# Performance work log

Measured on AMD Instinct MI355X. Metric: run time of the kernel, lower is better.

Reference implementation:

```python
import jax, jax.numpy as jnp
import numpy as np

B, T, I, H, O = 32, 2048, 12, 512, 3
L = 3  # GRU layers


def _gru_layer(x_seq, h0, w_ih, w_hh, b_ih, b_hh):
    # x_seq: [B,T,D], h0: [B,H]; PyTorch gate order: r, z, n
    xW = jnp.einsum('btd,gd->btg', x_seq, w_ih) + b_ih  # [B,T,3H]

    def step(h, xw_t):
        hw = h @ w_hh.T + b_hh                  # [B,3H]
        xr, xz, xn = jnp.split(xw_t, 3, axis=-1)
        hr, hz, hn = jnp.split(hw, 3, axis=-1)
        r = jax.nn.sigmoid(xr + hr)
        z = jax.nn.sigmoid(xz + hz)
        n = jnp.tanh(xn + r * hn)
        h_new = (1.0 - z) * n + z * h
        return h_new, h_new

    h_last, ys = jax.lax.scan(step, h0, jnp.swapaxes(xW, 0, 1))  # ys: [T,B,H]
    return jnp.swapaxes(ys, 0, 1), h_last


def _prelu(x, a):
    return jnp.where(x >= 0, x, a * x)


def setup_inputs() -> dict:
    key = jax.random.key(0)
    ks = jax.random.split(key, 40)
    s = 1.0 / np.sqrt(H)

    def u(k, shape):
        return jax.random.uniform(k, shape, jnp.float32, -s, s)

    inp = {
        'x': jax.random.normal(ks[0], (B, T, I), jnp.float32),
        'vel_init': jax.random.normal(ks[1], (B, 1, 3), jnp.float32),
    }
    in_dims = [I, H, H]
    for l in range(L):
        inp[f'w_ih_{l}'] = u(ks[2 + 4 * l], (3 * H, in_dims[l]))
        inp[f'w_hh_{l}'] = u(ks[3 + 4 * l], (3 * H, H))
        inp[f'b_ih_{l}'] = u(ks[4 + 4 * l], (3 * H,))
        inp[f'b_hh_{l}'] = u(ks[5 + 4 * l], (3 * H,))
    inp['a1'] = jnp.array([0.25], jnp.float32)  # PReLU (single shared param)
    inp['dec_in_w'] = u(ks[14], (H, I)); inp['dec_in_b'] = u(ks[15], (H,))
    inp['vd0_w'] = u(ks[16], (H, 3)); inp['vd0_b'] = u(ks[17], (H,))
    inp['vd1_w'] = u(ks[18], (H, 3)); inp['vd1_b'] = u(ks[19], (H,))
    inp['vd2_w'] = u(ks[20], (H, 3)); inp['vd2_b'] = u(ks[21], (H,))
    inp['vel_w'] = u(ks[22], (O, H)); inp['vel_b'] = u(ks[23], (O,))
    inp['std_w'] = u(ks[24], (O, H)); inp['std_b'] = u(ks[25], (O,))
    inp['attn_w'] = u(ks[26], (1, H)); inp['attn_b'] = u(ks[27], (1,))
    return inp


def reference(x, vel_init, w_ih_0, w_hh_0, b_ih_0, b_hh_0,
              w_ih_1, w_hh_1, b_ih_1, b_hh_1,
              w_ih_2, w_hh_2, b_ih_2, b_hh_2,
              a1, dec_in_w, dec_in_b,
              vd0_w, vd0_b, vd1_w, vd1_b, vd2_w, vd2_b,
              vel_w, vel_b, std_w, std_b, attn_w, attn_b):
    v0 = vel_init[:, 0, :]  # [B,3]
    # h0 per layer from velocity decoders (permute(1,0,2)+cat -> layer axis)
    h0s = [v0 @ vd0_w.T + vd0_b, v0 @ vd1_w.T + vd1_b, v0 @ vd2_w.T + vd2_b]
    w_ih = [w_ih_0, w_ih_1, w_ih_2]
    w_hh = [w_hh_0, w_hh_1, w_hh_2]
    b_ih = [b_ih_0, b_ih_1, b_ih_2]
    b_hh = [b_hh_0, b_hh_1, b_hh_2]

    out = x
    for l in range(L):
        out, _ = _gru_layer(out, h0s[l], w_ih[l], w_hh[l], b_ih[l], b_hh[l])

    out = _prelu(out, a1)
    # softmax skip-attention over time dim
    scores = jnp.einsum('bth,oh->bto', out, attn_w) + attn_b      # [B,T,1]
    attn = jax.nn.softmax(scores, axis=1)
    out = out + attn * (jnp.einsum('bti,hi->bth', x, dec_in_w) + dec_in_b)

    vel = jnp.einsum('bth,oh->bto', out, vel_w) + vel_b
    std = jnp.einsum('bth,oh->bto', out, std_w) + std_b
    return vel, std
```

## Files before the change

### kernel.cpp

```cpp
#include <hip/hip_runtime.h>
#include <stdint.h>


#define B_ 32
#define T_ 2048
#define H_ 512
#define R_ 128

typedef __attribute__((ext_vector_type(8))) short s8v;
typedef __attribute__((ext_vector_type(4))) float f4v;
typedef __attribute__((ext_vector_type(4))) uint32_t u32x4;
typedef __attribute__((ext_vector_type(2))) unsigned short u16x2;

__device__ __forceinline__ uint16_t f2bf(float f){ return __builtin_bit_cast(uint16_t, (__bf16)f); }
__device__ __forceinline__ float bf2f(uint16_t b){ return __builtin_bit_cast(float, ((uint32_t)b)<<16); }

__device__ __forceinline__ s8v pack8(const float* f){
  s8v r;
  #pragma unroll
  for (int i=0;i<8;++i) r[i] = (short)f2bf(f[i]);
  return r;
}
__device__ __forceinline__ f4v mfma16(s8v a, s8v b, f4v c){
  return __builtin_amdgcn_mfma_f32_16x16x32_bf16(a,b,c,0,0,0);
}
#if __has_builtin(__builtin_amdgcn_rcpf)
__device__ __forceinline__ float rcp_(float x){ return __builtin_amdgcn_rcpf(x); }
#else
__device__ __forceinline__ float rcp_(float x){ return 1.0f/x; }
#endif
__device__ __forceinline__ float sigm(float s){ return rcp_(1.f + __expf(-s)); }
__device__ __forceinline__ float tanh2(float v){ return 1.f - 2.f*rcp_(1.f + __expf(2.f*v)); }

__device__ __forceinline__ u32x4 load_x4_sc(const void* p){
  u32x4 r;
  asm volatile("global_load_dwordx4 %0, %1, off sc0 sc1" : "=v"(r) : "v"(p) : "memory");
  return r;
}
__device__ __forceinline__ u32x4 load_x4_sc_wait(const void* p){
  u32x4 r;
  asm volatile("global_load_dwordx4 %0, %1, off sc0 sc1\n\ts_waitcnt vmcnt(0)"
               : "=v"(r) : "v"(p) : "memory");
  return r;
}
__device__ __forceinline__ uint32_t load_u32_sc_wait(const void* p){
  uint32_t r;
  asm volatile("global_load_dword %0, %1, off sc0 sc1\n\ts_waitcnt vmcnt(0)"
               : "=v"(r) : "v"(p) : "memory");
  return r;
}
__device__ __forceinline__ void store_s16_sc(void* p, uint32_t v){
  asm volatile("global_store_short %0, %1, off sc0 sc1" :: "v"(p), "v"(v) : "memory");
}
__device__ __forceinline__ void store_u32_sc(void* p, uint32_t v){
  asm volatile("global_store_dword %0, %1, off sc0 sc1" :: "v"(p), "v"(v) : "memory");
}

__device__ __forceinline__ bool chunk_ok(u32x4 c){
  u16x2 m = __builtin_bit_cast(u16x2, c[0]);
  m = __builtin_elementwise_max(m, __builtin_bit_cast(u16x2, c[1]));
  m = __builtin_elementwise_max(m, __builtin_bit_cast(u16x2, c[2]));
  m = __builtin_elementwise_max(m, __builtin_bit_cast(u16x2, c[3]));
  unsigned short mm = (m[0] > m[1]) ? m[0] : m[1];
  return mm != (unsigned short)0xFFFFu;
}
__device__ __forceinline__ bool valid16(const u32x4* a){
  u16x2 m = {0, 0};
  #pragma unroll
  for (int c=0;c<16;++c){
    #pragma unroll
    for (int i=0;i<4;++i)
      m = __builtin_elementwise_max(m, __builtin_bit_cast(u16x2, a[c][i]));
  }
  unsigned short mm = (m[0] > m[1]) ? m[0] : m[1];
  return mm != (unsigned short)0xFFFFu;
}

__global__ void poison_kernel(uint32_t* p, unsigned int n16)
{
  u32x4 v = {0xFFFFFFFFu, 0xFFFFFFFFu, 0xFFFFFFFFu, 0xFFFFFFFFu};
  for (unsigned int k = blockIdx.x*blockDim.x + threadIdx.x; k < n16;
       k += gridDim.x*blockDim.x)
    ((u32x4*)p)[k] = v;
}

__global__ void init_kernel(const float* __restrict__ vel_init,
    const float* __restrict__ w0, const float* __restrict__ b0,
    const float* __restrict__ w1, const float* __restrict__ b1,
    const float* __restrict__ w2, const float* __restrict__ b2,
    float* __restrict__ h0f, uint16_t* __restrict__ h0b, uint32_t* progress)
{
  const int l = blockIdx.x, tid = threadIdx.x;
  const float* w  = (l==0)?w0:((l==1)?w1:w2);
  const float* bb = (l==0)?b0:((l==1)?b1:b2);
  for (int idx = tid; idx < B_*H_; idx += 256){
    int b = idx >> 9, j = idx & 511;
    float s = bb[j] + vel_init[b*3+0]*w[j*3+0] + vel_init[b*3+1]*w[j*3+1]
                    + vel_init[b*3+2]*w[j*3+2];
    h0f[(size_t)l*(B_*H_) + idx] = s;
    h0b[(size_t)l*(B_*H_) + idx] = f2bf(s);
  }
  if (l == 0 && tid < 192) progress[tid] = 0;
}

struct ScanParams {
  const float* x;
  const float* wih[3];
  const float* whh[3];
  const float* bih[3];
  const float* bhh[3];
  const float* h0f;
  const uint16_t* h0b;
  uint16_t* ring0;
  uint16_t* ring1;
  uint16_t* out2;
  uint32_t* progress;
};

__global__ __launch_bounds__(128, 1) void fused_scan(ScanParams P)
{
  const int tid  = threadIdx.x;
  const int lane = tid & 63;
  const int mt   = tid >> 6;
  const int wgid = blockIdx.x;
  const int layer = wgid >> 5;
  const int wg   = wgid & 31;
  const int j0   = wg * 16;
  const int u    = lane & 15;
  const int lq   = lane >> 4;
  const int ko   = lq * 8;
  const int bd   = lq * 4;

  __shared__ uint16_t lds[48*512];

  const float* wih = P.wih[layer];
  const float* whh = P.whh[layer];
  const float* bih = P.bih[layer];
  const float* bhh = P.bhh[layer];

  const float bs0 = bih[0*H_ + j0 + u] + bhh[0*H_ + j0 + u];
  const float bs1 = bih[1*H_ + j0 + u] + bhh[1*H_ + j0 + u];
  const float bi2 = bih[2*H_ + j0 + u];
  const float bh2 = bhh[2*H_ + j0 + u];

  s8v whhf[3][16];
  #pragma unroll
  for (int nt=0; nt<3; ++nt){
    #pragma unroll
    for (int ks=0; ks<16; ++ks){
      const float* wp = whh + (size_t)(nt*H_ + j0 + u)*H_ + ks*32 + ko;
      float tmp[8];
      #pragma unroll
      for (int i=0;i<8;++i) tmp[i] = wp[i];
      whhf[nt][ks] = pack8(tmp);
    }
  }

  s8v w0f[3];
  if (layer == 0){
    #pragma unroll
    for (int nt=0; nt<3; ++nt){
      float tmp[8];
      #pragma unroll
      for (int i=0;i<8;++i){
        int k = ko + i;
        tmp[i] = (k < 12) ? wih[(size_t)(nt*H_ + j0 + u)*12 + k] : 0.f;
      }
      w0f[nt] = pack8(tmp);
    }
  } else {
    for (int e = tid; e < (48*512)/8; e += 128) {
      int idx = e * 8;
      int g = idx >> 9, k = idx & 511;
      const float* wp = wih + (size_t)((g>>4)*H_ + j0 + (g&15))*H_ + k;
      float tmp[8];
      #pragma unroll
      for (int i=0;i<8;++i) tmp[i] = wp[i];
      s8v v = pack8(tmp);
      uint32_t msk = (uint32_t)((((g&7) ^ (((g>>3)&1)<<1))) << 4);
      uint32_t off = (uint32_t)g*1024u + ((((uint32_t)k)*2u) ^ msk);
      *(u32x4*)((char*)lds + off) = __builtin_bit_cast(u32x4, v);
    }
  }
  __syncthreads();

  const uint16_t* inring = (layer==1) ? P.ring0 : P.ring1;
  uint16_t* outbuf = (layer==0) ? P.ring0 : ((layer==1) ? P.ring1 : P.out2);
  const bool outlin = (layer == 2);
  uint32_t* myprog = P.progress + layer*64 + wg*2 + mt;
  const uint32_t* nextprog = (layer<2) ? (P.progress + (layer+1)*64) : nullptr;

  float hold[4];
  #pragma unroll
  for (int r=0;r<4;++r)
    hold[r] = P.h0f[(size_t)layer*(B_*H_) + (size_t)(mt*16 + bd + r)*H_ + j0 + u];

  const uint32_t sw  = (uint32_t)((((u&7) ^ (((u>>3)&1)<<1))) << 4);
  const uint32_t gb0 = (uint32_t)((0*16 + u) * 1024);
  const uint32_t gb1 = (uint32_t)((1*16 + u) * 1024);
  const uint32_t gb2 = (uint32_t)((2*16 + u) * 1024);
  const uint32_t koB = (uint32_t)(ko * 2);
  const int cl = lane & 31;

  int poison_until = R_/2 - 4;

  for (int t = 0; t < T_; ++t) {
    f4v ac0 = {0,0,0,0}, ac1 = {0,0,0,0}, axn = {0,0,0,0}, ahn = {0,0,0,0};

    if (layer == 0) {
      const float* xp = P.x + ((size_t)(mt*16 + u)*T_ + (size_t)t)*12;
      float4 lo  = *(const float4*)(xp);
      float4 md  = *(const float4*)(xp + 4);
      float4 hi4 = *(const float4*)(xp + 8);
      float xv[8];
      xv[0] = (ko==0) ? lo.x : hi4.x;  xv[1] = (ko==0) ? lo.y : hi4.y;
      xv[2] = (ko==0) ? lo.z : hi4.z;  xv[3] = (ko==0) ? lo.w : hi4.w;
      xv[4] = (ko==0) ? md.x : 0.f;    xv[5] = (ko==0) ? md.y : 0.f;
      xv[6] = (ko==0) ? md.z : 0.f;    xv[7] = (ko==0) ? md.w : 0.f;
      s8v a = pack8(xv);
      ac0 = mfma16(a, w0f[0], ac0);
      ac1 = mfma16(a, w0f[1], ac1);
      axn = mfma16(a, w0f[2], axn);
    } else {
      const uint16_t* xslot = inring + (size_t)(t & (R_-1))*(B_*H_);
      const uint16_t* xin  = xslot + (size_t)(mt*16+u)*H_ + ko;
      const uint16_t* xcan = xslot + (size_t)(mt*16)*H_ + cl*16;
      u32x4 xa[16];
      while (1) {
        #pragma unroll
        for (int ks=0; ks<16; ++ks) xa[ks] = load_x4_sc(xin + ks*32);
        asm volatile("s_waitcnt vmcnt(0)" ::: "memory");
        __builtin_amdgcn_sched_barrier(0);
        if (__ballot(valid16(xa)) == ~0ull) break;
        while (1) {
          u32x4 c = load_x4_sc_wait(xcan);
          if (__ballot(chunk_ok(c)) == ~0ull) break;
          __builtin_amdgcn_s_sleep(2);
        }
      }
      #pragma unroll
      for (int ks=0; ks<16; ++ks){
        s8v a = __builtin_bit_cast(s8v, xa[ks]);
        uint32_t kk = ((uint32_t)(ks*64) + koB) ^ sw;
        s8v w0 = *(const s8v*)((const char*)lds + gb0 + kk);
        s8v w1 = *(const s8v*)((const char*)lds + gb1 + kk);
        s8v w2 = *(const s8v*)((const char*)lds + gb2 + kk);
        ac0 = mfma16(a, w0, ac0);
        ac1 = mfma16(a, w1, ac1);
        axn = mfma16(a, w2, axn);
      }
    }

    const uint16_t* hslot = (t == 0)
        ? (P.h0b + (size_t)layer*(B_*H_))
        : (outlin ? (P.out2 + (size_t)(t-1)*(B_*H_))
                  : (outbuf + (size_t)((t-1) & (R_-1))*(B_*H_)));
    const uint16_t* hp   = hslot + (size_t)(mt*16+u)*H_ + ko;
    const uint16_t* hcan = hslot + (size_t)(mt*16)*H_ + cl*16;
    u32x4 ha[16];
    while (1) {
      #pragma unroll
      for (int ks=0; ks<16; ++ks) ha[ks] = load_x4_sc(hp + ks*32);
      asm volatile("s_waitcnt vmcnt(0)" ::: "memory");
      __builtin_amdgcn_sched_barrier(0);
      if (t == 0) break;
      if (__ballot(valid16(ha)) == ~0ull) break;
      while (1) {
        u32x4 c = load_x4_sc_wait(hcan);
        if (__ballot(chunk_ok(c)) == ~0ull) break;
        __builtin_amdgcn_s_sleep(2);
      }
    }
    #pragma unroll
    for (int ks=0; ks<16; ++ks){
      s8v a = __builtin_bit_cast(s8v, ha[ks]);
      ac0 = mfma16(a, whhf[0][ks], ac0);
      ac1 = mfma16(a, whhf[1][ks], ac1);
      ahn = mfma16(a, whhf[2][ks], ahn);
    }

    uint16_t* orow = outbuf
        + (outlin ? (size_t)t*(B_*H_) : (size_t)(t & (R_-1))*(B_*H_))
        + (size_t)(mt*16 + bd)*H_ + j0 + u;
    #pragma unroll
    for (int r=0;r<4;++r){
      float rg = sigm(ac0[r] + bs0);
      float zg = sigm(ac1[r] + bs1);
      float ng = tanh2(axn[r] + bi2 + rg*(ahn[r] + bh2));
      float hv = ng + zg*(hold[r] - ng);
      hold[r] = hv;
      store_s16_sc(orow + (size_t)r*H_, (uint32_t)f2bf(hv));
    }

    if (layer > 0 && (t & 15) == 15 && lane == 0)
      store_u32_sc(myprog, (uint32_t)t);

    if (layer < 2 && t >= R_/2) {
      if (t > poison_until) {
        while (1) {
          int c = (int)load_u32_sc_wait(nextprog + lane);
          #pragma unroll
          for (int off=32; off>0; off>>=1){
            int c2 = __shfl_xor(c, off, 64);
            c = (c2 < c) ? c2 : c;
          }
          poison_until = c + R_/2 - 4;
          if (t <= poison_until) break;
          __builtin_amdgcn_s_sleep(8);
        }
      }
      int sp = (t + R_/2) & (R_-1);
      uint16_t* prow = outbuf + (size_t)sp*(B_*H_) + (size_t)(mt*16 + bd)*H_ + j0 + u;
      #pragma unroll
      for (int r=0;r<4;++r) store_s16_sc(prow + (size_t)r*H_, 0xFFFFu);
    }
  }
}

__global__ void scores_kernel(const uint16_t* __restrict__ out2,
    const float* __restrict__ attn_w, const float* __restrict__ attn_b,
    const float* __restrict__ a1, float* __restrict__ scores)
{
  int gw = (blockIdx.x * blockDim.x + threadIdx.x) >> 6;
  int lane = threadIdx.x & 63;
  int b = gw >> 11, t = gw & 2047;
  float alpha = a1[0];
  u32x4 q = *(const u32x4*)(out2 + ((size_t)t*B_ + b)*H_ + lane*8);
  const uint16_t* ob = (const uint16_t*)&q;
  const float* aw = attn_w + lane*8;
  float acc = 0.f;
  #pragma unroll
  for (int i=0;i<8;++i){
    float ov = bf2f(ob[i]);
    ov = (ov >= 0.f) ? ov : alpha*ov;
    acc += ov * aw[i];
  }
  #pragma unroll
  for (int off=32; off>0; off>>=1) acc += __shfl_xor(acc, off, 64);
  if (lane == 0) scores[(size_t)b*T_ + t] = acc + attn_b[0];
}

__global__ void softmax_kernel(const float* __restrict__ scores, float* __restrict__ attn)
{
  int b = blockIdx.x, tid = threadIdx.x;
  __shared__ float red[256];
  const float* row = scores + (size_t)b*T_;
  float v[8]; float m = -3.4e38f;
  #pragma unroll
  for (int i=0;i<8;++i){ v[i] = row[tid + i*256]; m = fmaxf(m, v[i]); }
  red[tid] = m; __syncthreads();
  for (int s=128; s>0; s>>=1){ if (tid < s) red[tid] = fmaxf(red[tid], red[tid+s]); __syncthreads(); }
  m = red[0]; __syncthreads();
  float sum = 0.f;
  #pragma unroll
  for (int i=0;i<8;++i){ v[i] = __expf(v[i]-m); sum += v[i]; }
  red[tid] = sum; __syncthreads();
  for (int s=128; s>0; s>>=1){ if (tid < s) red[tid] += red[tid+s]; __syncthreads(); }
  float inv = 1.f / red[0];
  #pragma unroll
  for (int i=0;i<8;++i) attn[(size_t)b*T_ + tid + i*256] = v[i]*inv;
}

__global__ void final_kernel(const uint16_t* __restrict__ out2, const float* __restrict__ x,
    const float* __restrict__ attn, const float* __restrict__ dw, const float* __restrict__ db,
    const float* __restrict__ vw, const float* __restrict__ vb,
    const float* __restrict__ swt, const float* __restrict__ sb,
    const float* __restrict__ a1, float* __restrict__ dout)
{
  int gw = (blockIdx.x * blockDim.x + threadIdx.x) >> 6;
  int lane = threadIdx.x & 63;
  int b = gw >> 11, t = gw & 2047;
  float alpha = a1[0];
  u32x4 q = *(const u32x4*)(out2 + ((size_t)t*B_ + b)*H_ + lane*8);
  const uint16_t* ob = (const uint16_t*)&q;
  const float* xp = x + ((size_t)b*T_ + t)*12;
  float xr[12];
  #pragma unroll
  for (int i=0;i<12;++i) xr[i] = xp[i];
  float av = attn[(size_t)b*T_ + t];
  float acc[6] = {0,0,0,0,0,0};
  #pragma unroll
  for (int k=0;k<8;++k){
    int j = lane*8 + k;
    float ov = bf2f(ob[k]);
    ov = (ov >= 0.f) ? ov : alpha*ov;
    float d = db[j];
    const float* dwp = dw + (size_t)j*12;
    #pragma unroll
    for (int i=0;i<12;++i) d += xr[i]*dwp[i];
    float uo = ov + av*d;
    #pragma unroll
    for (int o=0;o<3;++o){
      acc[o]   += uo * vw[(size_t)o*H_ + j];
      acc[3+o] += uo * swt[(size_t)o*H_ + j];
    }
  }
  #pragma unroll
  for (int o=0;o<6;++o){
    #pragma unroll
    for (int off=32; off>0; off>>=1) acc[o] += __shfl_xor(acc[o], off, 64);
  }
  if (lane == 0){
    size_t p = ((size_t)b*T_ + t)*3;
    #pragma unroll
    for (int o=0;o<3;++o){
      dout[p + o] = acc[o] + vb[o];
      dout[(size_t)B_*T_*3 + p + o] = acc[3+o] + sb[o];
    }
  }
}

extern "C" void kernel_launch(void* const* d_in, const int* in_sizes, int n_in,
                              void* d_out, int out_size, void* d_ws, size_t ws_size,
                              hipStream_t stream)
{
  (void)in_sizes; (void)n_in; (void)out_size; (void)ws_size;
  const float* x        = (const float*)d_in[0];
  const float* vel_init = (const float*)d_in[1];
  const float* w_ih[3] = {(const float*)d_in[2], (const float*)d_in[6],  (const float*)d_in[10]};
  const float* w_hh[3] = {(const float*)d_in[3], (const float*)d_in[7],  (const float*)d_in[11]};
  const float* b_ih[3] = {(const float*)d_in[4], (const float*)d_in[8],  (const float*)d_in[12]};
  const float* b_hh[3] = {(const float*)d_in[5], (const float*)d_in[9],  (const float*)d_in[13]};
  const float* a1     = (const float*)d_in[14];
  const float* dec_w  = (const float*)d_in[15];
  const float* dec_b  = (const float*)d_in[16];
  const float* vd_w[3] = {(const float*)d_in[17], (const float*)d_in[19], (const float*)d_in[21]};
  const float* vd_b[3] = {(const float*)d_in[18], (const float*)d_in[20], (const float*)d_in[22]};
  const float* vel_w  = (const float*)d_in[23];
  const float* vel_b  = (const float*)d_in[24];
  const float* std_w  = (const float*)d_in[25];
  const float* std_b  = (const float*)d_in[26];
  const float* attn_w = (const float*)d_in[27];
  const float* attn_b = (const float*)d_in[28];

  char* ws = (char*)d_ws;
  uint16_t* out2   = (uint16_t*)(ws);
  uint16_t* ring0  = (uint16_t*)(ws + (size_t)67108864);
  uint16_t* ring1  = (uint16_t*)(ws + (size_t)71303168);
  float*    h0f    = (float*)   (ws + (size_t)75497472);
  uint16_t* h0b    = (uint16_t*)(ws + (size_t)75694080);
  float*    scores = (float*)   (ws + (size_t)75792384);
  float*    attnp  = (float*)   (ws + (size_t)76054528);
  uint32_t* progress = (uint32_t*)(ws + (size_t)76316672);

  poison_kernel<<<2048, 256, 0, stream>>>((uint32_t*)ws, 72u*1024u*1024u/16u);
  init_kernel<<<3, 256, 0, stream>>>(vel_init, vd_w[0], vd_b[0], vd_w[1], vd_b[1],
                                     vd_w[2], vd_b[2], h0f, h0b, progress);

  ScanParams P;
  P.x = x;
  for (int l=0;l<3;++l){ P.wih[l]=w_ih[l]; P.whh[l]=w_hh[l]; P.bih[l]=b_ih[l]; P.bhh[l]=b_hh[l]; }
  P.h0f = h0f; P.h0b = h0b;
  P.ring0 = ring0; P.ring1 = ring1; P.out2 = out2; P.progress = progress;

  fused_scan<<<96, 128, 0, stream>>>(P);

  scores_kernel<<<(B_*T_)/4, 256, 0, stream>>>(out2, attn_w, attn_b, a1, scores);
  softmax_kernel<<<B_, 256, 0, stream>>>(scores, attnp);
  final_kernel<<<(B_*T_)/4, 256, 0, stream>>>(out2, x, attnp, dec_w, dec_b,
                                              vel_w, vel_b, std_w, std_b, a1, (float*)d_out);
}
```

Baseline: 8.427 ms.

## Pin each GRU layer to its own XCD and use L2-scoped recurrent exchange

Launches extra workgroups and has each one read its XCC id and claim a layer slot through atomics, so that all 32 workgroups of a layer share one XCD. When every layer lands on its home XCD, the per-step hidden-state exchange uses an 8-deep ring with L2-scoped (sc0) loads and stores instead of system-coherent ones. The next timestep's input activations are also prefetched during the current step. Surplus workgroups exit early. The cost is a startup claim/barrier phase, reliance on XCC placement, and a spin fallback to coherent loads if workgroups end up off their home XCD.

New measurement: 8.520 ms. Within noise of the previous version (+1.1%).

```diff
diff --git a/kernel.cpp b/kernel.cpp
--- a/kernel.cpp
+++ b/kernel.cpp
@@ -6,6 +6,7 @@
 #define T_ 2048
 #define H_ 512
 #define R_ 128
+#define HR_ 8
 
 typedef __attribute__((ext_vector_type(8))) short s8v;
 typedef __attribute__((ext_vector_type(4))) float f4v;
@@ -55,6 +56,24 @@
 __device__ __forceinline__ void store_u32_sc(void* p, uint32_t v){
   asm volatile("global_store_dword %0, %1, off sc0 sc1" :: "v"(p), "v"(v) : "memory");
 }
+__device__ __forceinline__ u32x4 load_x4_l2(const void* p){
+  u32x4 r;
+  asm volatile("global_load_dwordx4 %0, %1, off sc0" : "=v"(r) : "v"(p) : "memory");
+  return r;
+}
+__device__ __forceinline__ void store_s16_l2(void* p, uint32_t v){
+  asm volatile("global_store_short %0, %1, off sc0" :: "v"(p), "v"(v) : "memory");
+}
+
+__device__ __forceinline__ void load16(u32x4* a, const uint16_t* base, bool l2){
+  if (l2) {
+    #pragma unroll
+    for (int ks=0; ks<16; ++ks) a[ks] = load_x4_l2(base + ks*32);
+  } else {
+    #pragma unroll
+    for (int ks=0; ks<16; ++ks) a[ks] = load_x4_sc(base + ks*32);
+  }
+}
 
 __device__ __forceinline__ bool chunk_ok(u32x4 c){
   u16x2 m = __builtin_bit_cast(u16x2, c[0]);
@@ -76,6 +95,17 @@
   return mm != (unsigned short)0xFFFFu;
 }
 
+__device__ __forceinline__ uint32_t get_xcc(){
+  uint32_t x;
+  asm volatile("s_getreg_b32 %0, hwreg(HW_REG_XCC_ID)" : "=s"(x));
+  return x & 7u;
+}
+__device__ __forceinline__ uint64_t realtime_(){
+  uint64_t t;
+  asm volatile("s_memrealtime %0\n\ts_waitcnt lgkmcnt(0)" : "=s"(t));
+  return t;
+}
+
 __global__ void poison_kernel(uint32_t* p, unsigned int n16)
 {
   u32x4 v = {0xFFFFFFFFu, 0xFFFFFFFFu, 0xFFFFFFFFu, 0xFFFFFFFFu};
@@ -88,7 +118,8 @@
     const float* __restrict__ w0, const float* __restrict__ b0,
     const float* __restrict__ w1, const float* __restrict__ b1,
     const float* __restrict__ w2, const float* __restrict__ b2,
-    float* __restrict__ h0f, uint16_t* __restrict__ h0b, uint32_t* progress)
+    float* __restrict__ h0f, uint16_t* __restrict__ h0b,
+    uint32_t* progress, uint32_t* claimp)
 {
   const int l = blockIdx.x, tid = threadIdx.x;
   const float* w  = (l==0)?w0:((l==1)?w1:w2);
@@ -101,6 +132,7 @@
     h0b[(size_t)l*(B_*H_) + idx] = f2bf(s);
   }
   if (l == 0 && tid < 192) progress[tid] = 0;
+  if (l == 0 && tid >= 192 && tid < 200) claimp[tid-192] = 0;
 }
 
 struct ScanParams {
@@ -111,10 +143,13 @@
   const float* bhh[3];
   const float* h0f;
   const uint16_t* h0b;
-  uint16_t* ring0;
-  uint16_t* ring1;
+  uint16_t* xr0;
+  uint16_t* xr1;
+  uint16_t* hr0;
+  uint16_t* hr1;
   uint16_t* out2;
   uint32_t* progress;
+  uint32_t* claimp;
 };
 
 __global__ __launch_bounds__(128, 1) void fused_scan(ScanParams P)
@@ -122,16 +157,59 @@
   const int tid  = threadIdx.x;
   const int lane = tid & 63;
   const int mt   = tid >> 6;
-  const int wgid = blockIdx.x;
-  const int layer = wgid >> 5;
-  const int wg   = wgid & 31;
-  const int j0   = wg * 16;
   const int u    = lane & 15;
   const int lq   = lane >> 4;
   const int ko   = lq * 8;
   const int bd   = lq * 4;
 
   __shared__ uint16_t lds[48*512];
+  __shared__ char pad_[36864];
+  __shared__ int sh_role[3];
+  if (P.x == nullptr) ((volatile char*)pad_)[0] = 1;
+
+  if (tid == 0){
+    int layer = -1, wg = -1, home = 0;
+    uint32_t xcc = get_xcc();
+    if (xcc < 3u){
+      unsigned s = atomicAdd(&P.claimp[xcc], 1u);
+      if (s < 32u){ layer = (int)xcc; wg = (int)s; home = 1; }
+    }
+    if (layer < 0){
+      uint64_t t0 = realtime_();
+      while (realtime_() - t0 < 5000ull) __builtin_amdgcn_s_sleep(32);
+      for (;;){
+        bool allfull = true;
+        for (int l=0; l<3 && layer<0; ++l){
+          if (__hip_atomic_load(&P.claimp[l], __ATOMIC_RELAXED,
+                                __HIP_MEMORY_SCOPE_AGENT) < 32u){
+            allfull = false;
+            unsigned s = atomicAdd(&P.claimp[l], 1u);
+            if (s < 32u){ layer = l; wg = (int)s; home = (xcc == (uint32_t)l); }
+          }
+        }
+        if (layer >= 0 || allfull) break;
+        __builtin_amdgcn_s_sleep(16);
+      }
+    }
+    int fast = 0;
+    if (layer >= 0){
+      if (!home) atomicAdd(&P.claimp[4], 1u);
+      __hip_atomic_fetch_add(&P.claimp[3], 1u, __ATOMIC_ACQ_REL,
+                             __HIP_MEMORY_SCOPE_AGENT);
+      while (__hip_atomic_load(&P.claimp[3], __ATOMIC_ACQUIRE,
+                               __HIP_MEMORY_SCOPE_AGENT) < 96u)
+        __builtin_amdgcn_s_sleep(8);
+      fast = (__hip_atomic_load(&P.claimp[4], __ATOMIC_ACQUIRE,
+                                __HIP_MEMORY_SCOPE_AGENT) == 0u) ? 1 : 0;
+    }
+    sh_role[0] = layer; sh_role[1] = wg; sh_role[2] = fast;
+  }
+  __syncthreads();
+  const int layer = sh_role[0];
+  if (layer < 0) return;
+  const int wg = sh_role[1];
+  const bool fastmode = (sh_role[2] != 0);
+  const int j0 = wg * 16;
 
   const float* wih = P.wih[layer];
   const float* whh = P.whh[layer];
@@ -184,9 +262,9 @@
   }
   __syncthreads();
 
-  const uint16_t* inring = (layer==1) ? P.ring0 : P.ring1;
-  uint16_t* outbuf = (layer==0) ? P.ring0 : ((layer==1) ? P.ring1 : P.out2);
-  const bool outlin = (layer == 2);
+  const uint16_t* inring = (layer==1) ? P.xr0 : P.xr1;
+  uint16_t* hring = (layer==0) ? P.hr0 : P.hr1;
+  uint16_t* xout  = (layer==0) ? P.xr0 : P.xr1;
   uint32_t* myprog = P.progress + layer*64 + wg*2 + mt;
   const uint32_t* nextprog = (layer<2) ? (P.progress + (layer+1)*64) : nullptr;
 
@@ -201,11 +279,49 @@
   const uint32_t gb2 = (uint32_t)((2*16 + u) * 1024);
   const uint32_t koB = (uint32_t)(ko * 2);
   const int cl = lane & 31;
-
-  int poison_until = R_/2 - 4;
+  const size_t rowoff = (size_t)(mt*16 + bd)*H_ + j0 + u;
+
+  bool hfast = fastmode;
+  int poison_until = 63;
+
+  u32x4 xa[16];
+  auto issue_x = [&](int tt){
+    const uint16_t* xin = inring + (size_t)(tt & (R_-1))*(B_*H_)
+                          + (size_t)(mt*16+u)*H_ + ko;
+    #pragma unroll
+    for (int ks=0; ks<16; ++ks) xa[ks] = load_x4_sc(xin + ks*32);
+  };
+  if (layer > 0) issue_x(0);
 
   for (int t = 0; t < T_; ++t) {
     f4v ac0 = {0,0,0,0}, ac1 = {0,0,0,0}, axn = {0,0,0,0}, ahn = {0,0,0,0};
+
+    if (layer > 0) {
+      asm volatile("s_waitcnt vmcnt(0)" ::: "memory");
+      __builtin_amdgcn_sched_barrier(0);
+      if (__ballot(valid16(xa)) != ~0ull) {
+        const uint16_t* xslot = inring + (size_t)(t & (R_-1))*(B_*H_);
+        const uint16_t* xcan  = xslot + (size_t)(mt*16)*H_ + cl*16;
+        do {
+          while (1) {
+            u32x4 c = load_x4_sc_wait(xcan);
+            if (__ballot(chunk_ok(c)) == ~0ull) break;
+            __builtin_amdgcn_s_sleep(2);
+          }
+          issue_x(t);
+          asm volatile("s_waitcnt vmcnt(0)" ::: "memory");
+          __builtin_amdgcn_sched_barrier(0);
+        } while (__ballot(valid16(xa)) != ~0ull);
+      }
+    }
+
+    const uint16_t* hsrc = (t == 0)
+        ? (P.h0b + (size_t)layer*(B_*H_))
+        : (layer == 2 ? (P.out2 + (size_t)(t-1)*(B_*H_))
+                      : (hring + (size_t)((t-1) & (HR_-1))*(B_*H_)));
+    const uint16_t* hp = hsrc + (size_t)(mt*16+u)*H_ + ko;
+    u32x4 ha[16];
+    load16(ha, hp, hfast);
 
     if (layer == 0) {
       const float* xp = P.x + ((size_t)(mt*16 + u)*T_ + (size_t)t)*12;
@@ -222,22 +338,6 @@
       ac1 = mfma16(a, w0f[1], ac1);
       axn = mfma16(a, w0f[2], axn);
     } else {
-      const uint16_t* xslot = inring + (size_t)(t & (R_-1))*(B_*H_);
-      const uint16_t* xin  = xslot + (size_t)(mt*16+u)*H_ + ko;
-      const uint16_t* xcan = xslot + (size_t)(mt*16)*H_ + cl*16;
-      u32x4 xa[16];
-      while (1) {
-        #pragma unroll
-        for (int ks=0; ks<16; ++ks) xa[ks] = load_x4_sc(xin + ks*32);
-        asm volatile("s_waitcnt vmcnt(0)" ::: "memory");
-        __builtin_amdgcn_sched_barrier(0);
-        if (__ballot(valid16(xa)) == ~0ull) break;
-        while (1) {
-          u32x4 c = load_x4_sc_wait(xcan);
-          if (__ballot(chunk_ok(c)) == ~0ull) break;
-          __builtin_amdgcn_s_sleep(2);
-        }
-      }
       #pragma unroll
       for (int ks=0; ks<16; ++ks){
         s8v a = __builtin_bit_cast(s8v, xa[ks]);
@@ -251,26 +351,19 @@
       }
     }
 
-    const uint16_t* hslot = (t == 0)
-        ? (P.h0b + (size_t)layer*(B_*H_))
-        : (outlin ? (P.out2 + (size_t)(t-1)*(B_*H_))
-                  : (outbuf + (size_t)((t-1) & (R_-1))*(B_*H_)));
-    const uint16_t* hp   = hslot + (size_t)(mt*16+u)*H_ + ko;
-    const uint16_t* hcan = hslot + (size_t)(mt*16)*H_ + cl*16;
-    u32x4 ha[16];
-    while (1) {
-      #pragma unroll
-      for (int ks=0; ks<16; ++ks) ha[ks] = load_x4_sc(hp + ks*32);
-      asm volatile("s_waitcnt vmcnt(0)" ::: "memory");
-      __builtin_amdgcn_sched_barrier(0);
-      if (t == 0) break;
-      if (__ballot(valid16(ha)) == ~0ull) break;
-      while (1) {
-        u32x4 c = load_x4_sc_wait(hcan);
-        if (__ballot(chunk_ok(c)) == ~0ull) break;
-        __builtin_amdgcn_s_sleep(2);
-      }
-    }
+    asm volatile("s_waitcnt vmcnt(0)" ::: "memory");
+    __builtin_amdgcn_sched_barrier(0);
+    if (t > 0) {
+      int spins = 0;
+      while (__ballot(valid16(ha)) != ~0ull) {
+        if (++spins > 512) hfast = false;
+        __builtin_amdgcn_s_sleep(1);
+        load16(ha, hp, hfast);
+        asm volatile("s_waitcnt vmcnt(0)" ::: "memory");
+        __builtin_amdgcn_sched_barrier(0);
+      }
+    }
+
     #pragma unroll
     for (int ks=0; ks<16; ++ks){
       s8v a = __builtin_bit_cast(s8v, ha[ks]);
@@ -279,23 +372,46 @@
       ahn = mfma16(a, whhf[2][ks], ahn);
     }
 
-    uint16_t* orow = outbuf
-        + (outlin ? (size_t)t*(B_*H_) : (size_t)(t & (R_-1))*(B_*H_))
-        + (size_t)(mt*16 + bd)*H_ + j0 + u;
-    #pragma unroll
-    for (int r=0;r<4;++r){
-      float rg = sigm(ac0[r] + bs0);
-      float zg = sigm(ac1[r] + bs1);
-      float ng = tanh2(axn[r] + bi2 + rg*(ahn[r] + bh2));
-      float hv = ng + zg*(hold[r] - ng);
-      hold[r] = hv;
-      store_s16_sc(orow + (size_t)r*H_, (uint32_t)f2bf(hv));
+    if (layer < 2) {
+      uint16_t* hrow = hring + (size_t)(t & (HR_-1))*(B_*H_) + rowoff;
+      uint16_t* xrow = xout  + (size_t)(t & (R_-1))*(B_*H_) + rowoff;
+      #pragma unroll
+      for (int r=0;r<4;++r){
+        float rg = sigm(ac0[r] + bs0);
+        float zg = sigm(ac1[r] + bs1);
+        float ng = tanh2(axn[r] + bi2 + rg*(ahn[r] + bh2));
+        float hv = ng + zg*(hold[r] - ng);
+        hold[r] = hv;
+        uint32_t bv = (uint32_t)f2bf(hv);
+        if (fastmode) store_s16_l2(hrow + (size_t)r*H_, bv);
+        else          store_s16_sc(hrow + (size_t)r*H_, bv);
+        store_s16_sc(xrow + (size_t)r*H_, bv);
+      }
+      uint16_t* prow = hring + (size_t)((t+4) & (HR_-1))*(B_*H_) + rowoff;
+      #pragma unroll
+      for (int r=0;r<4;++r){
+        if (fastmode) store_s16_l2(prow + (size_t)r*H_, 0xFFFFu);
+        else          store_s16_sc(prow + (size_t)r*H_, 0xFFFFu);
+      }
+    } else {
+      uint16_t* orow = P.out2 + (size_t)t*(B_*H_) + rowoff;
+      #pragma unroll
+      for (int r=0;r<4;++r){
+        float rg = sigm(ac0[r] + bs0);
+        float zg = sigm(ac1[r] + bs1);
+        float ng = tanh2(axn[r] + bi2 + rg*(ahn[r] + bh2));
+        float hv = ng + zg*(hold[r] - ng);
+        hold[r] = hv;
+        uint32_t bv = (uint32_t)f2bf(hv);
+        if (fastmode) store_s16_l2(orow + (size_t)r*H_, bv);
+        else          store_s16_sc(orow + (size_t)r*H_, bv);
+      }
     }
 
     if (layer > 0 && (t & 15) == 15 && lane == 0)
       store_u32_sc(myprog, (uint32_t)t);
 
-    if (layer < 2 && t >= R_/2) {
+    if (layer < 2 && t >= 64) {
       if (t > poison_until) {
         while (1) {
           int c = (int)load_u32_sc_wait(nextprog + lane);
@@ -304,16 +420,17 @@
             int c2 = __shfl_xor(c, off, 64);
             c = (c2 < c) ? c2 : c;
           }
-          poison_until = c + R_/2 - 4;
+          poison_until = c + 60;
           if (t <= poison_until) break;
           __builtin_amdgcn_s_sleep(8);
         }
       }
-      int sp = (t + R_/2) & (R_-1);
-      uint16_t* prow = outbuf + (size_t)sp*(B_*H_) + (size_t)(mt*16 + bd)*H_ + j0 + u;
-      #pragma unroll
-      for (int r=0;r<4;++r) store_s16_sc(prow + (size_t)r*H_, 0xFFFFu);
-    }
+      uint16_t* qrow = xout + (size_t)((t+64) & (R_-1))*(B_*H_) + rowoff;
+      #pragma unroll
+      for (int r=0;r<4;++r) store_s16_sc(qrow + (size_t)r*H_, 0xFFFFu);
+    }
+
+    if (layer > 0 && t+1 < T_) issue_x(t+1);
   }
 }
 
@@ -435,25 +552,29 @@
 
   char* ws = (char*)d_ws;
   uint16_t* out2   = (uint16_t*)(ws);
-  uint16_t* ring0  = (uint16_t*)(ws + (size_t)67108864);
-  uint16_t* ring1  = (uint16_t*)(ws + (size_t)71303168);
-  float*    h0f    = (float*)   (ws + (size_t)75497472);
-  uint16_t* h0b    = (uint16_t*)(ws + (size_t)75694080);
-  float*    scores = (float*)   (ws + (size_t)75792384);
-  float*    attnp  = (float*)   (ws + (size_t)76054528);
-  uint32_t* progress = (uint32_t*)(ws + (size_t)76316672);
-
-  poison_kernel<<<2048, 256, 0, stream>>>((uint32_t*)ws, 72u*1024u*1024u/16u);
+  uint16_t* xr0    = (uint16_t*)(ws + (size_t)67108864);
+  uint16_t* xr1    = (uint16_t*)(ws + (size_t)71303168);
+  uint16_t* hr0    = (uint16_t*)(ws + (size_t)75497472);
+  uint16_t* hr1    = (uint16_t*)(ws + (size_t)75759616);
+  float*    h0f    = (float*)   (ws + (size_t)76021760);
+  uint16_t* h0b    = (uint16_t*)(ws + (size_t)76218368);
+  float*    scores = (float*)   (ws + (size_t)76316672);
+  float*    attnp  = (float*)   (ws + (size_t)76578816);
+  uint32_t* progress = (uint32_t*)(ws + (size_t)76840960);
+  uint32_t* claimp   = (uint32_t*)(ws + (size_t)76841728);
+
+  poison_kernel<<<2048, 256, 0, stream>>>((uint32_t*)ws, 76021760u/16u);
   init_kernel<<<3, 256, 0, stream>>>(vel_init, vd_w[0], vd_b[0], vd_w[1], vd_b[1],
-                                     vd_w[2], vd_b[2], h0f, h0b, progress);
+                                     vd_w[2], vd_b[2], h0f, h0b, progress, claimp);
 
   ScanParams P;
   P.x = x;
   for (int l=0;l<3;++l){ P.wih[l]=w_ih[l]; P.whh[l]=w_hh[l]; P.bih[l]=b_ih[l]; P.bhh[l]=b_hh[l]; }
   P.h0f = h0f; P.h0b = h0b;
-  P.ring0 = ring0; P.ring1 = ring1; P.out2 = out2; P.progress = progress;
-
-  fused_scan<<<96, 128, 0, stream>>>(P);
+  P.xr0 = xr0; P.xr1 = xr1; P.hr0 = hr0; P.hr1 = hr1;
+  P.out2 = out2; P.progress = progress; P.claimp = claimp;
+
+  fused_scan<<<256, 128, 0, stream>>>(P);
 
   scores_kernel<<<(B_*T_)/4, 256, 0, stream>>>(out2, attn_w, attn_b, a1, scores);
   softmax_kernel<<<B_, 256, 0, stream>>>(scores, attnp);
```

## Prefetch next-step h/x loads speculatively and batch stores via LDS transpose

Applied to the files above, without the earlier changes.

Each step's h-state and layer-input loads are now issued right after the previous step's gates are computed, so they overlap with the output store and the poison and progress handling instead of starting at the top of the next step. The workgroup's own freshly computed h slice is merged from LDS so it does not wait on a global round trip. Outputs are transposed through a small LDS buffer so each lane writes one dwordx2 in place of four scattered 16-bit stores, and poison writes are batched the same way. The speculative loads may read not-yet-valid (poisoned) data and then fall back to the poll-and-reload path, which adds retry traffic when the prefetch runs ahead of the producers.

New measurement: 11.37 ms. +34.9%, slower.

```diff
diff --git a/kernel.cpp b/kernel.cpp
--- a/kernel.cpp
+++ b/kernel.cpp
@@ -6,10 +6,12 @@
 #define T_ 2048
 #define H_ 512
 #define R_ 128
+#define BH_ (B_*H_)
 
 typedef __attribute__((ext_vector_type(8))) short s8v;
 typedef __attribute__((ext_vector_type(4))) float f4v;
 typedef __attribute__((ext_vector_type(4))) uint32_t u32x4;
+typedef __attribute__((ext_vector_type(2))) uint32_t u32x2;
 typedef __attribute__((ext_vector_type(2))) unsigned short u16x2;
 
 __device__ __forceinline__ uint16_t f2bf(float f){ return __builtin_bit_cast(uint16_t, (__bf16)f); }
@@ -49,8 +51,8 @@
                : "=v"(r) : "v"(p) : "memory");
   return r;
 }
-__device__ __forceinline__ void store_s16_sc(void* p, uint32_t v){
-  asm volatile("global_store_short %0, %1, off sc0 sc1" :: "v"(p), "v"(v) : "memory");
+__device__ __forceinline__ void store_x2_sc(void* p, u32x2 v){
+  asm volatile("global_store_dwordx2 %0, %1, off sc0 sc1" :: "v"(p), "v"(v) : "memory");
 }
 __device__ __forceinline__ void store_u32_sc(void* p, uint32_t v){
   asm volatile("global_store_dword %0, %1, off sc0 sc1" :: "v"(p), "v"(v) : "memory");
@@ -97,8 +99,8 @@
     int b = idx >> 9, j = idx & 511;
     float s = bb[j] + vel_init[b*3+0]*w[j*3+0] + vel_init[b*3+1]*w[j*3+1]
                     + vel_init[b*3+2]*w[j*3+2];
-    h0f[(size_t)l*(B_*H_) + idx] = s;
-    h0b[(size_t)l*(B_*H_) + idx] = f2bf(s);
+    h0f[(size_t)l*BH_ + idx] = s;
+    h0b[(size_t)l*BH_ + idx] = f2bf(s);
   }
   if (l == 0 && tid < 192) progress[tid] = 0;
 }
@@ -132,6 +134,7 @@
   const int bd   = lq * 4;
 
   __shared__ uint16_t lds[48*512];
+  __shared__ uint16_t lds_t[2][2][16][16];
 
   const float* wih = P.wih[layer];
   const float* whh = P.whh[layer];
@@ -193,7 +196,7 @@
   float hold[4];
   #pragma unroll
   for (int r=0;r<4;++r)
-    hold[r] = P.h0f[(size_t)layer*(B_*H_) + (size_t)(mt*16 + bd + r)*H_ + j0 + u];
+    hold[r] = P.h0f[(size_t)layer*BH_ + (size_t)(mt*16 + bd + r)*H_ + j0 + u];
 
   const uint32_t sw  = (uint32_t)((((u&7) ^ (((u>>3)&1)<<1))) << 4);
   const uint32_t gb0 = (uint32_t)((0*16 + u) * 1024);
@@ -201,17 +204,54 @@
   const uint32_t gb2 = (uint32_t)((2*16 + u) * 1024);
   const uint32_t koB = (uint32_t)(ko * 2);
   const int cl = lane & 31;
+  const int sb = lane >> 2, sq = lane & 3;
+  const size_t wrow = (size_t)(mt*16 + sb)*H_ + j0 + sq*4;
+  const int ks0 = wg >> 1;
+  const bool ownseg = ((lq >> 1) == (wg & 1));
 
   int poison_until = R_/2 - 4;
 
+  u32x4 ha[16], xa[16], x0a[3];
+  const uint16_t* hp = P.h0b + (size_t)layer*BH_ + (size_t)(mt*16+u)*H_ + ko;
+
+  auto hload = [&](){
+    #pragma unroll
+    for (int ks=0; ks<16; ++ks) ha[ks] = load_x4_sc(hp + ks*32);
+  };
+  auto issue_x = [&](int tt){
+    const uint16_t* xin = inring + (size_t)(tt & (R_-1))*BH_
+                          + (size_t)(mt*16+u)*H_ + ko;
+    #pragma unroll
+    for (int ks=0; ks<16; ++ks) xa[ks] = load_x4_sc(xin + ks*32);
+  };
+  auto issue_x0 = [&](int tt){
+    const float* xp = P.x + ((size_t)(mt*16 + u)*T_ + (size_t)tt)*12;
+    x0a[0] = *(const u32x4*)(xp);
+    x0a[1] = *(const u32x4*)(xp + 4);
+    x0a[2] = *(const u32x4*)(xp + 8);
+  };
+  auto merge_own = [&](int p){
+    u32x4 own = *(const u32x4*)&lds_t[p][mt][u][(lq & 1) * 8];
+    if (ownseg) {
+      #pragma unroll
+      for (int ks=0; ks<16; ++ks)
+        if (ks == ks0) ha[ks] = own;
+    }
+  };
+
+  hload();
+  if (layer == 0) issue_x0(0); else issue_x(0);
+
   for (int t = 0; t < T_; ++t) {
+    asm volatile("s_waitcnt vmcnt(0)" ::: "memory");
+    __builtin_amdgcn_sched_barrier(0);
+
     f4v ac0 = {0,0,0,0}, ac1 = {0,0,0,0}, axn = {0,0,0,0}, ahn = {0,0,0,0};
 
     if (layer == 0) {
-      const float* xp = P.x + ((size_t)(mt*16 + u)*T_ + (size_t)t)*12;
-      float4 lo  = *(const float4*)(xp);
-      float4 md  = *(const float4*)(xp + 4);
-      float4 hi4 = *(const float4*)(xp + 8);
+      float4 lo  = __builtin_bit_cast(float4, x0a[0]);
+      float4 md  = __builtin_bit_cast(float4, x0a[1]);
+      float4 hi4 = __builtin_bit_cast(float4, x0a[2]);
       float xv[8];
       xv[0] = (ko==0) ? lo.x : hi4.x;  xv[1] = (ko==0) ? lo.y : hi4.y;
       xv[2] = (ko==0) ? lo.z : hi4.z;  xv[3] = (ko==0) ? lo.w : hi4.w;
@@ -222,21 +262,19 @@
       ac1 = mfma16(a, w0f[1], ac1);
       axn = mfma16(a, w0f[2], axn);
     } else {
-      const uint16_t* xslot = inring + (size_t)(t & (R_-1))*(B_*H_);
-      const uint16_t* xin  = xslot + (size_t)(mt*16+u)*H_ + ko;
-      const uint16_t* xcan = xslot + (size_t)(mt*16)*H_ + cl*16;
-      u32x4 xa[16];
-      while (1) {
-        #pragma unroll
-        for (int ks=0; ks<16; ++ks) xa[ks] = load_x4_sc(xin + ks*32);
-        asm volatile("s_waitcnt vmcnt(0)" ::: "memory");
-        __builtin_amdgcn_sched_barrier(0);
-        if (__ballot(valid16(xa)) == ~0ull) break;
-        while (1) {
-          u32x4 c = load_x4_sc_wait(xcan);
-          if (__ballot(chunk_ok(c)) == ~0ull) break;
-          __builtin_amdgcn_s_sleep(2);
-        }
+      if (__ballot(valid16(xa)) != ~0ull) {
+        const uint16_t* xslot = inring + (size_t)(t & (R_-1))*BH_;
+        const uint16_t* xcan  = xslot + (size_t)(mt*16)*H_ + cl*16;
+        do {
+          while (1) {
+            u32x4 c = load_x4_sc_wait(xcan);
+            if (__ballot(chunk_ok(c)) == ~0ull) break;
+            __builtin_amdgcn_s_sleep(2);
+          }
+          issue_x(t);
+          asm volatile("s_waitcnt vmcnt(0)" ::: "memory");
+          __builtin_amdgcn_sched_barrier(0);
+        } while (__ballot(valid16(xa)) != ~0ull);
       }
       #pragma unroll
       for (int ks=0; ks<16; ++ks){
@@ -251,24 +289,22 @@
       }
     }
 
-    const uint16_t* hslot = (t == 0)
-        ? (P.h0b + (size_t)layer*(B_*H_))
-        : (outlin ? (P.out2 + (size_t)(t-1)*(B_*H_))
-                  : (outbuf + (size_t)((t-1) & (R_-1))*(B_*H_)));
-    const uint16_t* hp   = hslot + (size_t)(mt*16+u)*H_ + ko;
-    const uint16_t* hcan = hslot + (size_t)(mt*16)*H_ + cl*16;
-    u32x4 ha[16];
-    while (1) {
-      #pragma unroll
-      for (int ks=0; ks<16; ++ks) ha[ks] = load_x4_sc(hp + ks*32);
-      asm volatile("s_waitcnt vmcnt(0)" ::: "memory");
-      __builtin_amdgcn_sched_barrier(0);
-      if (t == 0) break;
-      if (__ballot(valid16(ha)) == ~0ull) break;
-      while (1) {
-        u32x4 c = load_x4_sc_wait(hcan);
-        if (__ballot(chunk_ok(c)) == ~0ull) break;
-        __builtin_amdgcn_s_sleep(2);
+    if (t > 0) {
+      merge_own((t-1) & 1);
+      if (__ballot(valid16(ha)) != ~0ull) {
+        const uint16_t* hslot = hp - ((size_t)(mt*16+u)*H_ + ko);
+        const uint16_t* hcan  = hslot + (size_t)(mt*16)*H_ + cl*16;
+        do {
+          while (1) {
+            u32x4 c = load_x4_sc_wait(hcan);
+            if (__ballot(chunk_ok(c)) == ~0ull) break;
+            __builtin_amdgcn_s_sleep(2);
+          }
+          hload();
+          asm volatile("s_waitcnt vmcnt(0)" ::: "memory");
+          __builtin_amdgcn_sched_barrier(0);
+          merge_own((t-1) & 1);
+        } while (__ballot(valid16(ha)) != ~0ull);
       }
     }
     #pragma unroll
@@ -279,41 +315,54 @@
       ahn = mfma16(a, whhf[2][ks], ahn);
     }
 
-    uint16_t* orow = outbuf
-        + (outlin ? (size_t)t*(B_*H_) : (size_t)(t & (R_-1))*(B_*H_))
-        + (size_t)(mt*16 + bd)*H_ + j0 + u;
-    #pragma unroll
-    for (int r=0;r<4;++r){
-      float rg = sigm(ac0[r] + bs0);
-      float zg = sigm(ac1[r] + bs1);
-      float ng = tanh2(axn[r] + bi2 + rg*(ahn[r] + bh2));
-      float hv = ng + zg*(hold[r] - ng);
-      hold[r] = hv;
-      store_s16_sc(orow + (size_t)r*H_, (uint32_t)f2bf(hv));
+    {
+      const int p = t & 1;
+      #pragma unroll
+      for (int r=0;r<4;++r){
+        float rg = sigm(ac0[r] + bs0);
+        float zg = sigm(ac1[r] + bs1);
+        float ng = tanh2(axn[r] + bi2 + rg*(ahn[r] + bh2));
+        float hv = ng + zg*(hold[r] - ng);
+        hold[r] = hv;
+        lds_t[p][mt][bd + r][u] = f2bf(hv);
+      }
+    }
+    asm volatile("s_waitcnt lgkmcnt(0)" ::: "memory");
+    __builtin_amdgcn_sched_barrier(0);
+    u32x2 wv = *(const u32x2*)&lds_t[t & 1][mt][sb][sq * 4];
+
+    if (t + 1 < T_) {
+      hp = outbuf + (outlin ? (size_t)t*BH_ : (size_t)(t & (R_-1))*BH_)
+           + (size_t)(mt*16+u)*H_ + ko;
+      hload();
+      if (layer == 0) issue_x0(t + 1); else issue_x(t + 1);
+    }
+
+    {
+      uint16_t* drow = outbuf
+          + (outlin ? (size_t)t*BH_ : (size_t)(t & (R_-1))*BH_) + wrow;
+      store_x2_sc(drow, wv);
+      if (layer < 2 && t >= R_/2) {
+        if (t > poison_until) {
+          while (1) {
+            int c = (int)load_u32_sc_wait(nextprog + lane);
+            #pragma unroll
+            for (int off=32; off>0; off>>=1){
+              int c2 = __shfl_xor(c, off, 64);
+              c = (c2 < c) ? c2 : c;
+            }
+            poison_until = c + R_/2 - 4;
+            if (t <= poison_until) break;
+            __builtin_amdgcn_s_sleep(8);
+          }
+        }
+        u32x2 pz = {0xFFFFFFFFu, 0xFFFFFFFFu};
+        store_x2_sc(outbuf + (size_t)((t + R_/2) & (R_-1))*BH_ + wrow, pz);
+      }
     }
 
     if (layer > 0 && (t & 15) == 15 && lane == 0)
       store_u32_sc(myprog, (uint32_t)t);
-
-    if (layer < 2 && t >= R_/2) {
-      if (t > poison_until) {
-        while (1) {
-          int c = (int)load_u32_sc_wait(nextprog + lane);
-          #pragma unroll
-          for (int off=32; off>0; off>>=1){
-            int c2 = __shfl_xor(c, off, 64);
-            c = (c2 < c) ? c2 : c;
-          }
-          poison_until = c + R_/2 - 4;
-          if (t <= poison_until) break;
-          __builtin_amdgcn_s_sleep(8);
-        }
-      }
-      int sp = (t + R_/2) & (R_-1);
-      uint16_t* prow = outbuf + (size_t)sp*(B_*H_) + (size_t)(mt*16 + bd)*H_ + j0 + u;
-      #pragma unroll
-      for (int r=0;r<4;++r) store_s16_sc(prow + (size_t)r*H_, 0xFFFFu);
-    }
   }
 }
 
```
